# Optimization experiments

Hardware: AMD Instinct MI355X
Metric: run time of the kernel (lower is better)

Reference implementation:

```python
import jax, jax.numpy as jnp
import numpy as np

NFFT = 4_194_304
NMODES = 2
NTAPS = 101
GAMMA = 0.0016567  # [/W/m]
DZ = 80000.0       # [m]


def setup_inputs() -> dict:
    key = jax.random.key(0)
    k1, k2, k3 = jax.random.split(key, 3)
    xr = jax.random.normal(k1, (NFFT, NMODES), dtype=jnp.float32)
    xi = jax.random.normal(k2, (NFFT, NMODES), dtype=jnp.float32)
    # fconv1d kernel: [ntaps, in_features=Nmodes, out_features=Nmodes] (lecun_normal-ish scale)
    W = jax.random.normal(k3, (NTAPS, NMODES, NMODES), dtype=jnp.float32) / np.sqrt(NTAPS * NMODES)
    b = jnp.zeros((NMODES,), dtype=jnp.float32)
    power = jnp.zeros((1,), dtype=jnp.float32)  # 0 dBm
    return {"xr": xr, "xi": xi, "W": W, "b": b, "power": power}


def reference(xr, xi, W, b, power):
    # P = |x|^2, shape [Nfft, Nmodes]
    P = xr * xr + xi * xi
    # valid 1D conv over time: [Nfft, Nmodes] -> [Nfft - ntaps + 1, Nmodes]
    phi = jax.lax.conv_general_dilated(
        P[None],            # [1, Nfft, Nmodes]
        W,                  # [ntaps, in, out]
        window_strides=(1,),
        padding='VALID',
        dimension_numbers=('NWC', 'WIO', 'NWC'),
    )[0] + b                # [Nfft - ntaps + 1, Nmodes]

    nmodes = xr.shape[-1]
    scale = 0.001 * 10.0 ** (power[0] / 10.0) / nmodes  # dBm -> W, per mode
    n0 = NTAPS // 2
    x = (xr + 1j * xi)[n0:xr.shape[0] - n0]  # valid-conv aligned slice
    y = x * jnp.exp(-1j * phi * (GAMMA * scale * DZ))
    return y
```

## Files before the change

### kernel.cpp

```cpp
#include <hip/hip_runtime.h>
#include <hip/hip_bf16.h>

#define NFFT   4194304
#define NMODES 2
#define NTAPS  101
#define NVALID (NFFT - NTAPS + 1)
#define N0     (NTAPS / 2)

constexpr int BLOCK = 256;
constexpr int TILE  = 2048;
constexpr int NT    = (NVALID + TILE - 1) / TILE;
constexpr int WIN   = 2176;
constexpr int NM    = 15;
constexpr int TWRD  = 136;
constexpr int NTAB  = 8;

typedef __attribute__((ext_vector_type(8)))  short short8;
typedef __attribute__((ext_vector_type(16))) float float16;

static __device__ __forceinline__ unsigned short f2bf(float x) {
    __hip_bfloat16 h = __float2bfloat16(x);
    return *reinterpret_cast<unsigned short*>(&h);
}
static __device__ __forceinline__ unsigned pk(float e0, float e1) {
    return (unsigned)f2bf(e0) | ((unsigned)f2bf(e1) << 16);
}
static __device__ __forceinline__ int swz(int s) {
    return s ^ (((s >> 5) & 7) << 2);
}

__global__ __launch_bounds__(BLOCK, 8) void nl_kernel(
    const float* __restrict__ xa,
    const float* __restrict__ xb,
    const float* __restrict__ W,  const float* __restrict__ b,
    const float* __restrict__ power, unsigned* __restrict__ out)
{
    __shared__ __align__(16) unsigned Pl[WIN];
    __shared__ __align__(16) unsigned Bt[NTAB * TWRD];

    const int tid  = threadIdx.x;
    const int lane = tid & 63;
    const int wid  = tid >> 6;
    const int colc = lane & 31;
    const int h    = lane >> 5;
    const int cs   = colc >> 1;
    const int o    = colc & 1;
    const int r    = colc;

    const int tile_start = blockIdx.x * TILE;

    const float4* __restrict__ xa4 = reinterpret_cast<const float4*>(xa);
    const float4* __restrict__ xb4 = reinterpret_cast<const float4*>(xb);
    #pragma unroll
    for (int k = 0; k < 5; ++k) {
        const int s = 2 * tid + 512 * k;
        if (k < 4 || s < WIN) {
            const int g = tile_start + s;
            float4 a = make_float4(0.f, 0.f, 0.f, 0.f), c = a;
            if (g < NFFT) { a = xa4[g >> 1]; c = xb4[g >> 1]; }
            const unsigned u0 = pk(a.x * a.x + c.x * c.x, a.y * a.y + c.y * c.y);
            const unsigned u1 = pk(a.z * a.z + c.z * c.z, a.w * a.w + c.w * c.w);
            *reinterpret_cast<uint2*>(&Pl[swz(s)]) = make_uint2(u0, u1);
        }
    }

    __builtin_amdgcn_sched_barrier(0);

    {
        const float4* __restrict__ Wt = reinterpret_cast<const float4*>(W);
        for (int idx = tid; idx < NTAB * TWRD; idx += BLOCK) {
            const int tab = idx / TWRD;
            const int w   = idx - tab * TWRD;
            const int rr  = tab >> 1, oo = tab & 1;
            const int t   = (w & ~3) + rr + (w & 3) - 15;
            const bool ok = (unsigned)t <= 100u;
            const float4 ww = Wt[ok ? t : 0];
            Bt[idx] = ok ? pk(oo ? ww.y : ww.x, oo ? ww.w : ww.z) : 0u;
        }
    }
    __builtin_amdgcn_sched_barrier(0);
    __syncthreads();

    const int cb   = wid * 512;
    const int tau0 = 4 * h - cs + 15;
    const int tb   = (((tau0 & 3) << 1) | o) * TWRD + (tau0 >> 2) * 4;
    float16 acc = {};
    uint4 areg[4];
    #pragma unroll
    for (int m = 0; m < 4; ++m)
        areg[m] = *reinterpret_cast<const uint4*>(&Pl[swz(cb + 16 * r + 8 * m + 4 * h)]);
    #pragma unroll
    for (int m = 0; m < NM; ++m) {
        const uint4 bq = *reinterpret_cast<const uint4*>(&Bt[tb + 8 * m]);
        acc = __builtin_amdgcn_mfma_f32_32x32x16_bf16(
                  __builtin_bit_cast(short8, areg[m & 3]),
                  __builtin_bit_cast(short8, bq), acc, 0, 0, 0);
        if (m + 4 < NM)
            areg[m & 3] = *reinterpret_cast<const uint4*>(
                              &Pl[swz(cb + 16 * r + 8 * (m + 4) + 4 * h)]);
    }

    const float bo   = o ? b[1] : b[0];
    const float coef = 0.066268f * exp10f(power[0] * 0.1f);
    const int ibase  = 2 * (tile_start + cb + cs + N0) + o;
    const float* __restrict__ pxa = xa + ibase;
    const float* __restrict__ pxb = xb + ibase;
    unsigned* __restrict__ pou = out + (ibase - 2 * N0);

    if (blockIdx.x != NT - 1) {
        #pragma unroll
        for (int j = 0; j < 16; ++j) {
            const int off = 32 * ((j & 3) + 8 * (j >> 2) + 4 * h);
            const float Ax = pxa[off];
            const float Bx = pxb[off];
            float sn, cn;
            __sincosf((acc[j] + bo) * coef, &sn, &cn);
            __builtin_nontemporal_store(pk(Bx * cn - Ax * sn, Ax * cn + Bx * sn),
                                        &pou[off]);
        }
    } else {
        #pragma unroll
        for (int j = 0; j < 16; ++j) {
            const int row = (j & 3) + 8 * (j >> 2) + 4 * h;
            const int n   = tile_start + cb + 16 * row + cs;
            if (n < NVALID) {
                const float Ax = xa[(n + N0) * 2 + o];
                const float Bx = xb[(n + N0) * 2 + o];
                float sn, cn;
                __sincosf((acc[j] + bo) * coef, &sn, &cn);
                __builtin_nontemporal_store(pk(Bx * cn - Ax * sn, Ax * cn + Bx * sn),
                                            &out[n * 2 + o]);
            }
        }
    }
}

extern "C" void kernel_launch(void* const* d_in, const int* in_sizes, int n_in,
                              void* d_out, int out_size, void* d_ws, size_t ws_size,
                              hipStream_t stream) {
    const float* big[2] = {nullptr, nullptr};
    const float* W = nullptr; const float* b = nullptr; const float* power = nullptr;
    int nbig = 0;
    for (int i = 0; i < n_in; ++i) {
        const float* p = (const float*)d_in[i];
        const int sz = in_sizes[i];
        if (sz == NFFT * NMODES)       { if (nbig < 2) big[nbig++] = p; }
        else if (sz == NTAPS * NMODES * NMODES) { W = p; }
        else if (sz == NMODES)         { b = p; }
        else if (sz == 1)              { power = p; }
    }

    unsigned* out = (unsigned*)d_out;
    nl_kernel<<<NT, BLOCK, 0, stream>>>(big[0], big[1], W, b, power, out);
}
```

Baseline: 124.8 us.

## Stage conv results through LDS for coalesced vector epilogue loads and stores

The MFMA accumulator outputs are written to a swizzled LDS buffer and reread so each thread owns 8 contiguous samples. The x inputs can then be loaded as float4 ahead of time, overlapping the MFMA work, and outputs written as 16-byte nontemporal stores instead of scattered 4-byte ones. The prologue loads are also software-pipelined with two register sets, and launch bounds drop from 8 to 6 waves to leave room for the extra registers. This adds two block barriers and higher register pressure, which may cut occupancy.

```diff
diff --git a/kernel.cpp b/kernel.cpp
--- a/kernel.cpp
+++ b/kernel.cpp
@@ -17,6 +17,7 @@
 
 typedef __attribute__((ext_vector_type(8)))  short short8;
 typedef __attribute__((ext_vector_type(16))) float float16;
+typedef __attribute__((ext_vector_type(4)))  unsigned uintv4;
 
 static __device__ __forceinline__ unsigned short f2bf(float x) {
     __hip_bfloat16 h = __float2bfloat16(x);
@@ -29,14 +30,16 @@
     return s ^ (((s >> 5) & 7) << 2);
 }
 
-__global__ __launch_bounds__(BLOCK, 8) void nl_kernel(
+__global__ __launch_bounds__(BLOCK, 6) void nl_kernel(
     const float* __restrict__ xa,
     const float* __restrict__ xb,
     const float* __restrict__ W,  const float* __restrict__ b,
     const float* __restrict__ power, unsigned* __restrict__ out)
 {
-    __shared__ __align__(16) unsigned Pl[WIN];
-    __shared__ __align__(16) unsigned Bt[NTAB * TWRD];
+    __shared__ __align__(16) unsigned lds[4096];
+    unsigned* const Pl = lds;
+    unsigned* const Bt = lds + WIN;
+    float*    const Ph = reinterpret_cast<float*>(lds);
 
     const int tid  = threadIdx.x;
     const int lane = tid & 63;
@@ -51,18 +54,29 @@
 
     const float4* __restrict__ xa4 = reinterpret_cast<const float4*>(xa);
     const float4* __restrict__ xb4 = reinterpret_cast<const float4*>(xb);
-    #pragma unroll
-    for (int k = 0; k < 5; ++k) {
-        const int s = 2 * tid + 512 * k;
-        if (k < 4 || s < WIN) {
-            const int g = tile_start + s;
-            float4 a = make_float4(0.f, 0.f, 0.f, 0.f), c = a;
-            if (g < NFFT) { a = xa4[g >> 1]; c = xb4[g >> 1]; }
-            const unsigned u0 = pk(a.x * a.x + c.x * c.x, a.y * a.y + c.y * c.y);
-            const unsigned u1 = pk(a.z * a.z + c.z * c.z, a.w * a.w + c.w * c.w);
-            *reinterpret_cast<uint2*>(&Pl[swz(s)]) = make_uint2(u0, u1);
-        }
-    }
+
+    const float4 z4 = make_float4(0.f, 0.f, 0.f, 0.f);
+    #define LDK(k, A, C) { const int g = tile_start + 2 * tid + 512 * (k);          \
+        const bool v = (g < NFFT);                                                  \
+        A = v ? xa4[g >> 1] : z4; C = v ? xb4[g >> 1] : z4; }
+    #define STK(k, A, C) { const int s = 2 * tid + 512 * (k);                       \
+        const unsigned u0 = pk(A.x * A.x + C.x * C.x, A.y * A.y + C.y * C.y);       \
+        const unsigned u1 = pk(A.z * A.z + C.z * C.z, A.w * A.w + C.w * C.w);       \
+        *reinterpret_cast<uint2*>(&Pl[swz(s)]) = make_uint2(u0, u1); }
+    {
+        float4 a0, c0, a1, c1;
+        LDK(0, a0, c0); LDK(1, a1, c1);
+        STK(0, a0, c0); LDK(2, a0, c0);
+        STK(1, a1, c1); LDK(3, a1, c1);
+        STK(2, a0, c0);
+        const bool k4 = (2 * tid + 2048) < WIN;
+        float4 a4 = z4, c4 = z4;
+        if (k4) LDK(4, a4, c4);
+        STK(3, a1, c1);
+        if (k4) STK(4, a4, c4);
+    }
+    #undef LDK
+    #undef STK
 
     __builtin_amdgcn_sched_barrier(0);
 
@@ -100,38 +114,80 @@
                               &Pl[swz(cb + 16 * r + 8 * (m + 4) + 4 * h)]);
     }
 
-    const float bo   = o ? b[1] : b[0];
+    const int base  = tile_start + 8 * tid;
+    const bool full = (blockIdx.x != NT - 1);
+    float4 A0, A1, A2, A3, B0, B1, B2, B3;
+    if (full) {
+        const float4* __restrict__ pa = xa4 + ((base + N0) >> 1);
+        const float4* __restrict__ pb = xb4 + ((base + N0) >> 1);
+        A0 = pa[0]; A1 = pa[1]; A2 = pa[2]; A3 = pa[3];
+        B0 = pb[0]; B1 = pb[1]; B2 = pb[2]; B3 = pb[3];
+    }
+
+    const float bo = o ? b[1] : b[0];
+    __syncthreads();
+    #pragma unroll
+    for (int j = 0; j < 16; ++j) {
+        const int row = (j & 3) + 8 * (j >> 2) + 4 * h;
+        Ph[swz(wid * 1024 + 32 * row + colc)] = acc[j] + bo;
+    }
+    __syncthreads();
+
     const float coef = 0.066268f * exp10f(power[0] * 0.1f);
-    const int ibase  = 2 * (tile_start + cb + cs + N0) + o;
-    const float* __restrict__ pxa = xa + ibase;
-    const float* __restrict__ pxb = xb + ibase;
-    unsigned* __restrict__ pou = out + (ibase - 2 * N0);
-
-    if (blockIdx.x != NT - 1) {
-        #pragma unroll
-        for (int j = 0; j < 16; ++j) {
-            const int off = 32 * ((j & 3) + 8 * (j >> 2) + 4 * h);
-            const float Ax = pxa[off];
-            const float Bx = pxb[off];
-            float sn, cn;
-            __sincosf((acc[j] + bo) * coef, &sn, &cn);
-            __builtin_nontemporal_store(pk(Bx * cn - Ax * sn, Ax * cn + Bx * sn),
-                                        &pou[off]);
-        }
+    const float4 f0 = *reinterpret_cast<const float4*>(&Ph[swz(16 * tid +  0)]);
+    const float4 f1 = *reinterpret_cast<const float4*>(&Ph[swz(16 * tid +  4)]);
+    const float4 f2 = *reinterpret_cast<const float4*>(&Ph[swz(16 * tid +  8)]);
+    const float4 f3 = *reinterpret_cast<const float4*>(&Ph[swz(16 * tid + 12)]);
+
+    uintv4* __restrict__ out4 = reinterpret_cast<uintv4*>(out);
+
+    if (full) {
+        #define EPI(q, F, A, B) {                                                   \
+            float s00, c00, s01, c01, s10, c10, s11, c11;                           \
+            __sincosf(F.x * coef, &s00, &c00);                                      \
+            __sincosf(F.y * coef, &s01, &c01);                                      \
+            __sincosf(F.z * coef, &s10, &c10);                                      \
+            __sincosf(F.w * coef, &s11, &c11);                                      \
+            uintv4 ov;                                                              \
+            ov.x = pk(B.x * c00 - A.x * s00, A.x * c00 + B.x * s00);                \
+            ov.y = pk(B.y * c01 - A.y * s01, A.y * c01 + B.y * s01);                \
+            ov.z = pk(B.z * c10 - A.z * s10, A.z * c10 + B.z * s10);                \
+            ov.w = pk(B.w * c11 - A.w * s11, A.w * c11 + B.w * s11);                \
+            __builtin_nontemporal_store(ov, &out4[(base >> 1) + (q)]); }
+        EPI(0, f0, A0, B0)
+        EPI(1, f1, A1, B1)
+        EPI(2, f2, A2, B2)
+        EPI(3, f3, A3, B3)
+        #undef EPI
     } else {
-        #pragma unroll
-        for (int j = 0; j < 16; ++j) {
-            const int row = (j & 3) + 8 * (j >> 2) + 4 * h;
-            const int n   = tile_start + cb + 16 * row + cs;
-            if (n < NVALID) {
-                const float Ax = xa[(n + N0) * 2 + o];
-                const float Bx = xb[(n + N0) * 2 + o];
-                float sn, cn;
-                __sincosf((acc[j] + bo) * coef, &sn, &cn);
-                __builtin_nontemporal_store(pk(Bx * cn - Ax * sn, Ax * cn + Bx * sn),
-                                            &out[n * 2 + o]);
-            }
-        }
+        const float2* __restrict__ xa2 = reinterpret_cast<const float2*>(xa);
+        const float2* __restrict__ xb2 = reinterpret_cast<const float2*>(xb);
+        #define TEPI(q, p0v, p1v, p2v, p3v) {                                       \
+            const int n0v = base + 2 * (q);                                         \
+            if (n0v < NVALID) {                                                     \
+                const float2 Av = xa2[n0v + N0]; const float2 Bv = xb2[n0v + N0];   \
+                float s0, c0v, s1, c1v;                                             \
+                __sincosf((p0v) * coef, &s0, &c0v);                                 \
+                __sincosf((p1v) * coef, &s1, &c1v);                                 \
+                uint2 ov;                                                           \
+                ov.x = pk(Bv.x * c0v - Av.x * s0, Av.x * c0v + Bv.x * s0);          \
+                ov.y = pk(Bv.y * c1v - Av.y * s1, Av.y * c1v + Bv.y * s1);          \
+                reinterpret_cast<uint2*>(out)[n0v] = ov; }                          \
+            const int n1v = base + 2 * (q) + 1;                                     \
+            if (n1v < NVALID) {                                                     \
+                const float2 Av = xa2[n1v + N0]; const float2 Bv = xb2[n1v + N0];   \
+                float s0, c0v, s1, c1v;                                             \
+                __sincosf((p2v) * coef, &s0, &c0v);                                 \
+                __sincosf((p3v) * coef, &s1, &c1v);                                 \
+                uint2 ov;                                                           \
+                ov.x = pk(Bv.x * c0v - Av.x * s0, Av.x * c0v + Bv.x * s0);          \
+                ov.y = pk(Bv.y * c1v - Av.y * s1, Av.y * c1v + Bv.y * s1);          \
+                reinterpret_cast<uint2*>(out)[n1v] = ov; } }
+        TEPI(0, f0.x, f0.y, f0.z, f0.w)
+        TEPI(1, f1.x, f1.y, f1.z, f1.w)
+        TEPI(2, f2.x, f2.y, f2.z, f2.w)
+        TEPI(3, f3.x, f3.y, f3.z, f3.w)
+        #undef TEPI
     }
 }
 
```

Result: slower. 149.1 us (+19.5%).
